# Kernel tuning notes

Measured on AMD Instinct MI355X. Metric: run time of the kernel, lower is better.

The kernel has to match this reference:

```python
import jax, jax.numpy as jnp
import numpy as np

B, L, V, D_MODEL = 1, 2048, 32000, 768
N_LAYER, D_STATE, EXPAND, D_CONV = 2, 16, 2, 4
D_INNER = EXPAND * D_MODEL            # 1536
DT_RANK = -(-D_MODEL // D_STATE)      # ceil(768/16) = 48
EPS = 1e-5


def setup_inputs() -> dict:
    key = jax.random.key(0)
    ks = jax.random.split(key, 12)
    s = 0.02
    inp = {
        "input_ids": jax.random.randint(ks[0], (B, L), 0, V),
        "emb": jax.random.normal(ks[1], (V, D_MODEL), jnp.float32) * s,
        "norm_w": jnp.ones((N_LAYER, D_MODEL), jnp.float32),
        "in_proj_w": jax.random.normal(ks[2], (N_LAYER, D_MODEL, 2 * D_INNER), jnp.float32) * s,
        "conv_w": jax.random.normal(ks[3], (N_LAYER, D_INNER, 1, D_CONV), jnp.float32) * s,
        "conv_b": jnp.zeros((N_LAYER, D_INNER), jnp.float32),
        "x_proj_w": jax.random.normal(ks[4], (N_LAYER, D_INNER, DT_RANK + 2 * D_STATE), jnp.float32) * s,
        "dt_proj_w": jax.random.normal(ks[5], (N_LAYER, DT_RANK, D_INNER), jnp.float32) * s,
        "dt_proj_b": jax.random.normal(ks[6], (N_LAYER, D_INNER), jnp.float32) * s,
        "A_log": jnp.tile(jnp.log(jnp.arange(1, D_STATE + 1, dtype=jnp.float32)), (N_LAYER, D_INNER, 1)),
        "D": jnp.ones((N_LAYER, D_INNER), jnp.float32),
        "out_proj_w": jax.random.normal(ks[7], (N_LAYER, D_INNER, D_MODEL), jnp.float32) * s,
    }
    return inp


def _rmsnorm(x, w):
    return x * jax.lax.rsqrt(jnp.mean(x * x, axis=-1, keepdims=True) + EPS) * w


def _selective_scan(u, delta, A, Bm, Cm, D):
    # u, delta: (b,l,d); A: (d,n); Bm, Cm: (b,l,n); D: (d,)
    deltaA = jnp.exp(delta[..., None] * A)                     # (b,l,d,n)
    dBu = delta[..., None] * Bm[:, :, None, :] * u[..., None]  # (b,l,d,n)

    def comb(c1, c2):
        a1, b1 = c1
        a2, b2 = c2
        return a2 * a1, a2 * b1 + b2

    _, h = jax.lax.associative_scan(comb, (deltaA, dBu), axis=1)
    y = jnp.einsum('bldn,bln->bld', h, Cm)
    return y + u * D


def _mamba_block(x, in_proj_w, conv_w, conv_b, x_proj_w, dt_proj_w, dt_proj_b, A_log, D, out_proj_w):
    # x: (b,l,d_model)
    xz = x @ in_proj_w                                  # (b,l,2*d_inner)
    xr, res = jnp.split(xz, 2, axis=-1)
    # causal depthwise conv1d (left pad d_conv-1)
    xc = jax.lax.conv_general_dilated(
        jnp.swapaxes(xr, 1, 2), conv_w, (1,), [(D_CONV - 1, 0)],
        feature_group_count=D_INNER,
        dimension_numbers=('NCH', 'OIH', 'NCH'))
    xr = jax.nn.silu(jnp.swapaxes(xc + conv_b[:, None], 1, 2))  # (b,l,d_inner)

    A = -jnp.exp(A_log)                                 # (d_inner, n)
    x_dbl = xr @ x_proj_w                               # (b,l,dt_rank+2n)
    dt, Bm, Cm = jnp.split(x_dbl, [DT_RANK, DT_RANK + D_STATE], axis=-1)
    delta = jax.nn.softplus(dt @ dt_proj_w + dt_proj_b) # (b,l,d_inner)
    y = _selective_scan(xr, delta, A, Bm, Cm, D)
    return (y * jax.nn.silu(res)) @ out_proj_w


def reference(input_ids, emb, norm_w, in_proj_w, conv_w, conv_b, x_proj_w,
              dt_proj_w, dt_proj_b, A_log, D, out_proj_w):
    x = emb[input_ids]                                  # (b,l,d_model)
    for i in range(N_LAYER):
        x = x + _mamba_block(_rmsnorm(x, norm_w[i]), in_proj_w[i], conv_w[i],
                             conv_b[i], x_proj_w[i], dt_proj_w[i], dt_proj_b[i],
                             A_log[i], D[i], out_proj_w[i])
    return x
```

## Files before the change

kernel.cpp:

```cpp
#include <hip/hip_runtime.h>
#include <math.h>

#define L_SEQ 2048
#define DM    768
#define DI    1536
#define DTR   48
#define DST   16
#define XDW   80
#define NCH   64
#define LC    32
#define XPS   8
#define XPK   (DI / XPS)

typedef short bf16x8 __attribute__((ext_vector_type(8)));
typedef float f32x4  __attribute__((ext_vector_type(4)));

__device__ __forceinline__ float silu_f(float x) {
    return x / (1.0f + __expf(-x));
}

__device__ __forceinline__ short f2bf(float x) {
    union { float f; unsigned u; } v; v.f = x;
    unsigned r = v.u + 0x7fff + ((v.u >> 16) & 1);
    return (short)(r >> 16);
}

__device__ __forceinline__ float bf2f(short s) {
    union { float f; unsigned u; } v;
    v.u = ((unsigned)(unsigned short)s) << 16;
    return v.f;
}

__global__ __launch_bounds__(256) void prep_kernel(
    const int*   __restrict__ ids,
    const float* __restrict__ emb,
    const float* __restrict__ norm_w,
    const float* __restrict__ in_proj_w,
    const float* __restrict__ out_proj_w,
    const float* __restrict__ x_proj_w,
    float* __restrict__ x,
    short* __restrict__ xn_bf,
    short* __restrict__ ipw_t, short* __restrict__ opw_t, short* __restrict__ xpw_t)
{
    __shared__ float tile[32 * 33];
    __shared__ float wred[4];
    const int tid = threadIdx.x;

    {
        int row = blockIdx.x;
        int tok = ids[row];
        float4 v4 = make_float4(0.f, 0.f, 0.f, 0.f);
        if (tid < DM / 4) {
            v4 = ((const float4*)emb)[(size_t)tok * (DM / 4) + tid];
            ((float4*)x)[(size_t)row * (DM / 4) + tid] = v4;
        }
        float s = v4.x * v4.x + v4.y * v4.y + v4.z * v4.z + v4.w * v4.w;
        #pragma unroll
        for (int off = 32; off > 0; off >>= 1) s += __shfl_down(s, off, 64);
        int wave = tid >> 6, lane = tid & 63;
        if (lane == 0) wred[wave] = s;
        __syncthreads();
        float tot = wred[0] + wred[1] + wred[2] + wred[3];
        float rs = rsqrtf(tot / (float)DM + 1e-5f);
        if (tid < DM / 4) {
            int i = tid * 4;
            short4 o;
            o.x = f2bf(v4.x * rs * norm_w[i + 0]);
            o.y = f2bf(v4.y * rs * norm_w[i + 1]);
            o.z = f2bf(v4.z * rs * norm_w[i + 2]);
            o.w = f2bf(v4.w * rs * norm_w[i + 3]);
            ((short4*)xn_bf)[(size_t)row * (DM / 4) + tid] = o;
        }
        __syncthreads();
    }

    int lx = tid & 31, ly = tid >> 5;
    for (int t = blockIdx.x; t < 7200; t += gridDim.x) {
        int layer = t >= 3600;
        int tt = t - layer * 3600;
        const float* src; short* dst; int K, N, txc;
        if (tt < 2304) {
            src = in_proj_w + (size_t)layer * DM * 2 * DI;
            dst = ipw_t + (size_t)layer * 2 * DI * DM;
            K = DM; N = 2 * DI; txc = 96;
        } else if (tt < 3456) {
            tt -= 2304;
            src = out_proj_w + (size_t)layer * DI * DM;
            dst = opw_t + (size_t)layer * DM * DI;
            K = DI; N = DM; txc = 24;
        } else {
            tt -= 3456;
            src = x_proj_w + (size_t)layer * DI * XDW;
            dst = xpw_t + (size_t)layer * XDW * DI;
            K = DI; N = XDW; txc = 3;
        }
        int n0 = (tt % txc) * 32, k0 = (tt / txc) * 32;
        __syncthreads();
        #pragma unroll
        for (int i = 0; i < 4; i++) {
            int nn = n0 + lx;
            tile[(ly + i * 8) * 33 + lx] =
                (nn < N) ? src[(size_t)(k0 + ly + i * 8) * N + nn] : 0.f;
        }
        __syncthreads();
        #pragma unroll
        for (int i = 0; i < 4; i++) {
            int nn = n0 + ly + i * 8;
            if (nn < N)
                dst[(size_t)nn * K + k0 + lx] = f2bf(tile[lx * 33 + ly + i * 8]);
        }
    }
}

__global__ __launch_bounds__(256) void rmsnorm_kernel(
    const float* __restrict__ x, const float* __restrict__ w,
    short* __restrict__ out)
{
    int row = blockIdx.x;
    const float* xr = x + (size_t)row * DM;
    float s = 0.f;
    for (int i = threadIdx.x; i < DM; i += 256) { float v = xr[i]; s += v * v; }
    #pragma unroll
    for (int off = 32; off > 0; off >>= 1) s += __shfl_down(s, off, 64);
    __shared__ float ws[4];
    int wave = threadIdx.x >> 6, lane = threadIdx.x & 63;
    if (lane == 0) ws[wave] = s;
    __syncthreads();
    float tot = ws[0] + ws[1] + ws[2] + ws[3];
    float rs = rsqrtf(tot / (float)DM + 1e-5f);
    for (int i = threadIdx.x; i < DM; i += 256)
        out[(size_t)row * DM + i] = f2bf(xr[i] * rs * w[i]);
}

__global__ __launch_bounds__(256) void gemm_inproj(
    const short* __restrict__ A, const short* __restrict__ Bt,
    short* __restrict__ xcz_bf, short* __restrict__ res_bf, int M, int N, int K)
{
    __shared__ short As[128 * 32];
    __shared__ short Bs[128 * 32];
    int tid = threadIdx.x, lane = tid & 63, w = tid >> 6;
    int wr = w >> 1, wc = w & 1;
    int brow = blockIdx.y * 128, bcol = blockIdx.x * 128;

    f32x4 acc[4][4] = {};

    for (int k0 = 0; k0 < K; k0 += 32) {
        #pragma unroll
        for (int i = 0; i < 2; i++) {
            int c = tid + i * 256;
            int r = c >> 2, q = c & 3;
            const short* ga = A  + (size_t)(brow + r) * K + k0 + q * 8;
            const short* gb = Bt + (size_t)(bcol + r) * K + k0 + q * 8;
            __builtin_amdgcn_global_load_lds(
                (const __attribute__((address_space(1))) void*)ga,
                (__attribute__((address_space(3))) void*)&As[r * 32 + q * 8],
                16, 0, 0);
            __builtin_amdgcn_global_load_lds(
                (const __attribute__((address_space(1))) void*)gb,
                (__attribute__((address_space(3))) void*)&Bs[r * 32 + q * 8],
                16, 0, 0);
        }
        __syncthreads();

        bf16x8 af[4], bfv[4];
        int kh = (lane >> 4) * 8;
        int ml = lane & 15;
        #pragma unroll
        for (int t = 0; t < 4; t++) {
            af[t]  = *(const bf16x8*)&As[(wr * 64 + t * 16 + ml) * 32 + kh];
            bfv[t] = *(const bf16x8*)&Bs[(wc * 64 + t * 16 + ml) * 32 + kh];
        }
        #pragma unroll
        for (int mt = 0; mt < 4; mt++)
            #pragma unroll
            for (int nt = 0; nt < 4; nt++)
                acc[mt][nt] = __builtin_amdgcn_mfma_f32_16x16x32_bf16(
                    af[mt], bfv[nt], acc[mt][nt], 0, 0, 0);
        __syncthreads();
    }

    short* dst  = (bcol < DI) ? xcz_bf : res_bf;
    int    cofs = (bcol < DI) ? bcol : (bcol - DI);
    int r0 = (lane >> 4) * 4, c0 = lane & 15;
    #pragma unroll
    for (int mt = 0; mt < 4; mt++)
        #pragma unroll
        for (int nt = 0; nt < 4; nt++)
            #pragma unroll
            for (int reg = 0; reg < 4; reg++) {
                int row = brow + wr * 64 + mt * 16 + r0 + reg;
                int col = cofs + wc * 64 + nt * 16 + c0;
                dst[(size_t)row * DI + col] = f2bf(acc[mt][nt][reg]);
            }
}

__global__ __launch_bounds__(256) void gemm_bf16_bt_n64(
    const short* __restrict__ A, const short* __restrict__ Bt,
    float* __restrict__ C, int M, int N, int K)
{
    __shared__ short As[128 * 32];
    __shared__ short Bs[64 * 32];
    int tid = threadIdx.x, lane = tid & 63, w = tid >> 6;
    int brow = blockIdx.y * 128, bcol = blockIdx.x * 64;

    f32x4 acc[2][4] = {};

    for (int k0 = 0; k0 < K; k0 += 32) {
        #pragma unroll
        for (int i = 0; i < 2; i++) {
            int c = tid + i * 256;
            int r = c >> 2, q = c & 3;
            const short* ga = A + (size_t)(brow + r) * K + k0 + q * 8;
            __builtin_amdgcn_global_load_lds(
                (const __attribute__((address_space(1))) void*)ga,
                (__attribute__((address_space(3))) void*)&As[r * 32 + q * 8],
                16, 0, 0);
        }
        {
            int r = tid >> 2, q = tid & 3;
            const short* gb = Bt + (size_t)(bcol + r) * K + k0 + q * 8;
            __builtin_amdgcn_global_load_lds(
                (const __attribute__((address_space(1))) void*)gb,
                (__attribute__((address_space(3))) void*)&Bs[r * 32 + q * 8],
                16, 0, 0);
        }
        __syncthreads();

        bf16x8 af[2], bfv[4];
        int kh = (lane >> 4) * 8;
        int ml = lane & 15;
        #pragma unroll
        for (int mt = 0; mt < 2; mt++)
            af[mt] = *(const bf16x8*)&As[(w * 32 + mt * 16 + ml) * 32 + kh];
        #pragma unroll
        for (int nt = 0; nt < 4; nt++)
            bfv[nt] = *(const bf16x8*)&Bs[(nt * 16 + ml) * 32 + kh];
        #pragma unroll
        for (int mt = 0; mt < 2; mt++)
            #pragma unroll
            for (int nt = 0; nt < 4; nt++)
                acc[mt][nt] = __builtin_amdgcn_mfma_f32_16x16x32_bf16(
                    af[mt], bfv[nt], acc[mt][nt], 0, 0, 0);
        __syncthreads();
    }

    int r0 = (lane >> 4) * 4, c0 = lane & 15;
    #pragma unroll
    for (int mt = 0; mt < 2; mt++)
        #pragma unroll
        for (int nt = 0; nt < 4; nt++)
            #pragma unroll
            for (int reg = 0; reg < 4; reg++) {
                int row = brow + w * 32 + mt * 16 + r0 + reg;
                int col = bcol + nt * 16 + c0;
                C[(size_t)row * N + col] += acc[mt][nt][reg];
            }
}

__global__ __launch_bounds__(256) void conv_silu_kernel(
    const short* __restrict__ xcz_bf, const float* __restrict__ w,
    const float* __restrict__ b, short* __restrict__ xr_bf)
{
    int idx = blockIdx.x * 256 + threadIdx.x;
    if (idx >= L_SEQ * DI) return;
    int l = idx / DI, c = idx % DI;
    float4 wc = ((const float4*)w)[c];
    const short* col = xcz_bf + c;
    float acc = b[c];
    if (l >= 3) {
        acc += wc.x * bf2f(col[(size_t)(l - 3) * DI])
             + wc.y * bf2f(col[(size_t)(l - 2) * DI])
             + wc.z * bf2f(col[(size_t)(l - 1) * DI])
             + wc.w * bf2f(col[(size_t)l * DI]);
    } else {
        const float wv[4] = {wc.x, wc.y, wc.z, wc.w};
        for (int k = 0; k < 4; k++) {
            int ls = l - 3 + k;
            if (ls >= 0) acc += wv[k] * bf2f(col[(size_t)ls * DI]);
        }
    }
    xr_bf[idx] = f2bf(silu_f(acc));
}

__global__ __launch_bounds__(256) void xproj_splitk(
    const short* __restrict__ xr_bf,
    const short* __restrict__ xpw_t,
    float* __restrict__ part)
{
    int w = threadIdx.x >> 6, lane = threadIdx.x & 63;
    int r0 = blockIdx.x * 64 + w * 16;
    int k0 = blockIdx.y * XPK;
    int ml = lane & 15, kh = (lane >> 4) * 8;

    f32x4 acc[5] = {};
    for (int ks = 0; ks < XPK; ks += 32) {
        bf16x8 a = *(const bf16x8*)&xr_bf[(size_t)(r0 + ml) * DI + k0 + ks + kh];
        #pragma unroll
        for (int t = 0; t < 5; t++) {
            bf16x8 b = *(const bf16x8*)&xpw_t[(size_t)(t * 16 + ml) * DI + k0 + ks + kh];
            acc[t] = __builtin_amdgcn_mfma_f32_16x16x32_bf16(a, b, acc[t], 0, 0, 0);
        }
    }
    float* po = part + (size_t)blockIdx.y * L_SEQ * XDW;
    int r_base = r0 + (lane >> 4) * 4;
    #pragma unroll
    for (int t = 0; t < 5; t++)
        #pragma unroll
        for (int reg = 0; reg < 4; reg++)
            po[(size_t)(r_base + reg) * XDW + t * 16 + ml] = acc[t][reg];
}

__global__ __launch_bounds__(256) void dtproj_fused(
    const float* __restrict__ xpart, const float* __restrict__ dpw,
    const float* __restrict__ dpb, float* __restrict__ delta,
    float* __restrict__ xdbl_bc)
{
    __shared__ __align__(16) float As_f[16 * 68];
    __shared__ __align__(16) float Bs_f[16 * 68];
    int tid = threadIdx.x;
    int ty = tid >> 4, tx = tid & 15;
    int t = blockIdx.x;
    int bcol = (t % 24) * 64;
    int brow = (t / 24) * 64;

    float acc[4][4] = {};
    for (int k0 = 0; k0 < 48; k0 += 16) {
        __syncthreads();
        #pragma unroll
        for (int i = 0; i < 4; i++) {
            int idx = tid + i * 256;
            int m = idx >> 4, k = idx & 15;
            float s = 0.f;
            #pragma unroll
            for (int p = 0; p < XPS; p++)
                s += xpart[((size_t)p * L_SEQ + brow + m) * XDW + k0 + k];
            As_f[k * 68 + m] = s;
        }
        #pragma unroll
        for (int i = 0; i < 4; i++) {
            int idx = tid + i * 256;
            int k = idx >> 6, n = idx & 63;
            Bs_f[k * 68 + n] = dpw[(size_t)(k0 + k) * DI + bcol + n];
        }
        __syncthreads();
        #pragma unroll
        for (int k = 0; k < 16; k++) {
            float4 av = *(const float4*)&As_f[k * 68 + ty * 4];
            float4 bv = *(const float4*)&Bs_f[k * 68 + tx * 4];
            float a4[4] = {av.x, av.y, av.z, av.w};
            float b4[4] = {bv.x, bv.y, bv.z, bv.w};
            #pragma unroll
            for (int i = 0; i < 4; i++)
                #pragma unroll
                for (int jj = 0; jj < 4; jj++)
                    acc[i][jj] += a4[i] * b4[jj];
        }
    }
    #pragma unroll
    for (int i = 0; i < 4; i++) {
        int row = brow + ty * 4 + i;
        #pragma unroll
        for (int jj = 0; jj < 4; jj++) {
            int col = bcol + tx * 4 + jj;
            float v = acc[i][jj] + dpb[col];
            delta[(size_t)row * DI + col] = (v > 20.f) ? v : log1pf(__expf(v));
        }
    }
    if (t % 24 == 0) {
        for (int e = tid; e < 64 * 32; e += 256) {
            int r = e >> 5, cc = e & 31;
            float s = 0.f;
            #pragma unroll
            for (int p = 0; p < XPS; p++)
                s += xpart[((size_t)p * L_SEQ + brow + r) * XDW + DTR + cc];
            xdbl_bc[(size_t)(brow + r) * 32 + cc] = s;
        }
    }
}

__global__ __launch_bounds__(256) void scan_passA(
    const float* __restrict__ delta, const short* __restrict__ xr_bf,
    const float* __restrict__ xdbl_bc, const float* __restrict__ al,
    float* __restrict__ aprod, float* __restrict__ hfin)
{
    int d = blockIdx.x * 256 + threadIdx.x;
    int c = blockIdx.y;

    float Aloc[DST], h[DST], P[DST];
    #pragma unroll
    for (int n4 = 0; n4 < DST; n4 += 4) {
        float4 alv = *(const float4*)&al[(size_t)d * DST + n4];
        Aloc[n4 + 0] = -__expf(alv.x); Aloc[n4 + 1] = -__expf(alv.y);
        Aloc[n4 + 2] = -__expf(alv.z); Aloc[n4 + 3] = -__expf(alv.w);
    }
    #pragma unroll
    for (int n = 0; n < DST; n++) { h[n] = 0.f; P[n] = 1.f; }

    int l0 = c * LC;
    for (int l = l0; l < l0 + LC; l++) {
        float dl = delta[(size_t)l * DI + d];
        float ul = bf2f(xr_bf[(size_t)l * DI + d]);
        float du = dl * ul;
        float Bv[DST];
        const float4* B4 = (const float4*)(xdbl_bc + (size_t)l * 32);
        *(float4*)&Bv[0] = B4[0]; *(float4*)&Bv[4]  = B4[1];
        *(float4*)&Bv[8] = B4[2]; *(float4*)&Bv[12] = B4[3];
        #pragma unroll
        for (int n = 0; n < DST; n++) {
            float da = __expf(dl * Aloc[n]);
            h[n] = h[n] * da + du * Bv[n];
            P[n] *= da;
        }
    }
    size_t base = ((size_t)c * DI + d) * DST;
    #pragma unroll
    for (int n = 0; n < DST; n += 4) {
        *(float4*)&aprod[base + n] = *(float4*)&P[n];
        *(float4*)&hfin[base + n]  = *(float4*)&h[n];
    }
}

__global__ __launch_bounds__(256) void scan_passB(
    const float* __restrict__ aprod, const float* __restrict__ hfin,
    float* __restrict__ hin)
{
    int idx = blockIdx.x * 256 + threadIdx.x;
    if (idx >= DI * DST) return;
    float cur = 0.f;
    for (int c = 0; c < NCH; c++) {
        size_t o = (size_t)c * DI * DST + idx;
        hin[o] = cur;
        cur = hfin[o] + aprod[o] * cur;
    }
}

__global__ __launch_bounds__(256) void scan_passC(
    const float* __restrict__ delta, const short* __restrict__ xr_bf,
    const float* __restrict__ xdbl_bc, const float* __restrict__ al,
    const float* __restrict__ dpp, const float* __restrict__ hin,
    const short* __restrict__ res_bf, short* __restrict__ y2)
{
    int d = blockIdx.x * 256 + threadIdx.x;
    int c = blockIdx.y;

    float Aloc[DST], h[DST];
    #pragma unroll
    for (int n4 = 0; n4 < DST; n4 += 4) {
        float4 alv = *(const float4*)&al[(size_t)d * DST + n4];
        Aloc[n4 + 0] = -__expf(alv.x); Aloc[n4 + 1] = -__expf(alv.y);
        Aloc[n4 + 2] = -__expf(alv.z); Aloc[n4 + 3] = -__expf(alv.w);
    }
    size_t base = ((size_t)c * DI + d) * DST;
    #pragma unroll
    for (int n = 0; n < DST; n += 4)
        *(float4*)&h[n] = *(const float4*)&hin[base + n];
    float Dd = dpp[d];

    int l0 = c * LC;
    for (int l = l0; l < l0 + LC; l++) {
        float dl = delta[(size_t)l * DI + d];
        float ul = bf2f(xr_bf[(size_t)l * DI + d]);
        float du = dl * ul;
        float Bv[DST], Cv[DST];
        const float4* B4 = (const float4*)(xdbl_bc + (size_t)l * 32);
        const float4* C4 = (const float4*)(xdbl_bc + (size_t)l * 32 + 16);
        *(float4*)&Bv[0] = B4[0]; *(float4*)&Bv[4]  = B4[1];
        *(float4*)&Bv[8] = B4[2]; *(float4*)&Bv[12] = B4[3];
        *(float4*)&Cv[0] = C4[0]; *(float4*)&Cv[4]  = C4[1];
        *(float4*)&Cv[8] = C4[2]; *(float4*)&Cv[12] = C4[3];
        float y = 0.f;
        #pragma unroll
        for (int n = 0; n < DST; n++) {
            float da = __expf(dl * Aloc[n]);
            h[n] = h[n] * da + du * Bv[n];
            y += h[n] * Cv[n];
        }
        y += ul * Dd;
        float r = bf2f(res_bf[(size_t)l * DI + d]);
        y2[(size_t)l * DI + d] = f2bf(y * silu_f(r));
    }
}

extern "C" void kernel_launch(void* const* d_in, const int* in_sizes, int n_in,
                              void* d_out, int out_size, void* d_ws, size_t ws_size,
                              hipStream_t stream)
{
    const int*   ids       = (const int*)d_in[0];
    const float* emb       = (const float*)d_in[1];
    const float* norm_w    = (const float*)d_in[2];
    const float* in_proj_w = (const float*)d_in[3];
    const float* conv_w    = (const float*)d_in[4];
    const float* conv_b    = (const float*)d_in[5];
    const float* x_proj_w  = (const float*)d_in[6];
    const float* dt_proj_w = (const float*)d_in[7];
    const float* dt_proj_b = (const float*)d_in[8];
    const float* A_log     = (const float*)d_in[9];
    const float* Dp        = (const float*)d_in[10];
    const float* out_proj_w= (const float*)d_in[11];

    float* x = (float*)d_out;

    char* wsb = (char*)d_ws;
    auto alloc_f = [&](size_t n) { float* p = (float*)wsb; wsb += n * 4; return p; };
    auto alloc_s = [&](size_t n) { short* p = (short*)wsb; wsb += ((n * 2 + 15) & ~15ull); return p; };

    float* delta   = alloc_f((size_t)L_SEQ * DI);
    float* xpart   = alloc_f((size_t)XPS * L_SEQ * XDW);
    float* xdbl_bc = alloc_f((size_t)L_SEQ * 32);
    float* aprod   = alloc_f((size_t)NCH * DI * DST);
    float* hfin    = alloc_f((size_t)NCH * DI * DST);
    float* hin     = alloc_f((size_t)NCH * DI * DST);
    short* xcz_bf  = alloc_s((size_t)L_SEQ * DI);
    short* res_bf  = alloc_s((size_t)L_SEQ * DI);
    short* xn_bf   = alloc_s((size_t)L_SEQ * DM);
    short* y2_bf   = alloc_s((size_t)L_SEQ * DI);
    short* xr_bf   = alloc_s((size_t)L_SEQ * DI);
    short* ipw_t   = alloc_s((size_t)2 * 2 * DI * DM);
    short* opw_t   = alloc_s((size_t)2 * DM * DI);
    short* xpw_t   = alloc_s((size_t)2 * XDW * DI);

    prep_kernel<<<L_SEQ, 256, 0, stream>>>(
        ids, emb, norm_w, in_proj_w, out_proj_w, x_proj_w,
        x, xn_bf, ipw_t, opw_t, xpw_t);

    for (int layer = 0; layer < 2; layer++) {
        const float* nw   = norm_w    + (size_t)layer * DM;
        const float* cw   = conv_w    + (size_t)layer * DI * 4;
        const float* cb   = conv_b    + (size_t)layer * DI;
        const float* dpw  = dt_proj_w + (size_t)layer * DTR * DI;
        const float* dpb  = dt_proj_b + (size_t)layer * DI;
        const float* al   = A_log     + (size_t)layer * DI * DST;
        const float* dpp  = Dp        + (size_t)layer * DI;
        const short* ipwt = ipw_t + (size_t)layer * 2 * DI * DM;
        const short* opwt = opw_t + (size_t)layer * DM * DI;
        const short* xpwt = xpw_t + (size_t)layer * XDW * DI;

        if (layer == 1)
            rmsnorm_kernel<<<L_SEQ, 256, 0, stream>>>(x, nw, xn_bf);

        gemm_inproj<<<dim3(2 * DI / 128, L_SEQ / 128), 256, 0, stream>>>(
            xn_bf, ipwt, xcz_bf, res_bf, L_SEQ, 2 * DI, DM);

        conv_silu_kernel<<<(L_SEQ * DI) / 256, 256, 0, stream>>>(
            xcz_bf, cw, cb, xr_bf);

        xproj_splitk<<<dim3(L_SEQ / 64, XPS), 256, 0, stream>>>(xr_bf, xpwt, xpart);

        dtproj_fused<<<768, 256, 0, stream>>>(xpart, dpw, dpb, delta, xdbl_bc);

        scan_passA<<<dim3(DI / 256, NCH), 256, 0, stream>>>(
            delta, xr_bf, xdbl_bc, al, aprod, hfin);
        scan_passB<<<(DI * DST) / 256, 256, 0, stream>>>(aprod, hfin, hin);
        scan_passC<<<dim3(DI / 256, NCH), 256, 0, stream>>>(
            delta, xr_bf, xdbl_bc, al, dpp, hin, res_bf, y2_bf);

        gemm_bf16_bt_n64<<<dim3(DM / 64, L_SEQ / 128), 256, 0, stream>>>(
            y2_bf, opwt, x, L_SEQ, DM, DI);
    }
}
```

Measured before the change: 468.4 us.

## Shrink GEMM tiles, split-K out_proj with atomics, fold scan pass B into pass C

The in_proj GEMM now uses 128x64 tiles instead of 128x128, doubling its block count. The out_proj GEMM is split along K into two halves that accumulate into the residual with atomic adds, raising its parallelism from 192 blocks. The separate chunk-carry kernel (scan_passB) is removed: each pass C block recomputes its initial state by walking all earlier chunks' products and final states. This saves a launch and the hin buffer, but costs redundant O(NCH) reads per block and makes out_proj accumulation order nondeterministic.

```diff
diff --git a/kernel.cpp b/kernel.cpp
--- a/kernel.cpp
+++ b/kernel.cpp
@@ -132,71 +132,9 @@
         out[(size_t)row * DM + i] = f2bf(xr[i] * rs * w[i]);
 }
 
-__global__ __launch_bounds__(256) void gemm_inproj(
+__global__ __launch_bounds__(256) void gemm_inproj64(
     const short* __restrict__ A, const short* __restrict__ Bt,
     short* __restrict__ xcz_bf, short* __restrict__ res_bf, int M, int N, int K)
-{
-    __shared__ short As[128 * 32];
-    __shared__ short Bs[128 * 32];
-    int tid = threadIdx.x, lane = tid & 63, w = tid >> 6;
-    int wr = w >> 1, wc = w & 1;
-    int brow = blockIdx.y * 128, bcol = blockIdx.x * 128;
-
-    f32x4 acc[4][4] = {};
-
-    for (int k0 = 0; k0 < K; k0 += 32) {
-        #pragma unroll
-        for (int i = 0; i < 2; i++) {
-            int c = tid + i * 256;
-            int r = c >> 2, q = c & 3;
-            const short* ga = A  + (size_t)(brow + r) * K + k0 + q * 8;
-            const short* gb = Bt + (size_t)(bcol + r) * K + k0 + q * 8;
-            __builtin_amdgcn_global_load_lds(
-                (const __attribute__((address_space(1))) void*)ga,
-                (__attribute__((address_space(3))) void*)&As[r * 32 + q * 8],
-                16, 0, 0);
-            __builtin_amdgcn_global_load_lds(
-                (const __attribute__((address_space(1))) void*)gb,
-                (__attribute__((address_space(3))) void*)&Bs[r * 32 + q * 8],
-                16, 0, 0);
-        }
-        __syncthreads();
-
-        bf16x8 af[4], bfv[4];
-        int kh = (lane >> 4) * 8;
-        int ml = lane & 15;
-        #pragma unroll
-        for (int t = 0; t < 4; t++) {
-            af[t]  = *(const bf16x8*)&As[(wr * 64 + t * 16 + ml) * 32 + kh];
-            bfv[t] = *(const bf16x8*)&Bs[(wc * 64 + t * 16 + ml) * 32 + kh];
-        }
-        #pragma unroll
-        for (int mt = 0; mt < 4; mt++)
-            #pragma unroll
-            for (int nt = 0; nt < 4; nt++)
-                acc[mt][nt] = __builtin_amdgcn_mfma_f32_16x16x32_bf16(
-                    af[mt], bfv[nt], acc[mt][nt], 0, 0, 0);
-        __syncthreads();
-    }
-
-    short* dst  = (bcol < DI) ? xcz_bf : res_bf;
-    int    cofs = (bcol < DI) ? bcol : (bcol - DI);
-    int r0 = (lane >> 4) * 4, c0 = lane & 15;
-    #pragma unroll
-    for (int mt = 0; mt < 4; mt++)
-        #pragma unroll
-        for (int nt = 0; nt < 4; nt++)
-            #pragma unroll
-            for (int reg = 0; reg < 4; reg++) {
-                int row = brow + wr * 64 + mt * 16 + r0 + reg;
-                int col = cofs + wc * 64 + nt * 16 + c0;
-                dst[(size_t)row * DI + col] = f2bf(acc[mt][nt][reg]);
-            }
-}
-
-__global__ __launch_bounds__(256) void gemm_bf16_bt_n64(
-    const short* __restrict__ A, const short* __restrict__ Bt,
-    float* __restrict__ C, int M, int N, int K)
 {
     __shared__ short As[128 * 32];
     __shared__ short Bs[64 * 32];
@@ -244,6 +182,73 @@
         __syncthreads();
     }
 
+    short* dst  = (bcol < DI) ? xcz_bf : res_bf;
+    int    cofs = (bcol < DI) ? bcol : (bcol - DI);
+    int r0 = (lane >> 4) * 4, c0 = lane & 15;
+    #pragma unroll
+    for (int mt = 0; mt < 2; mt++)
+        #pragma unroll
+        for (int nt = 0; nt < 4; nt++)
+            #pragma unroll
+            for (int reg = 0; reg < 4; reg++) {
+                int row = brow + w * 32 + mt * 16 + r0 + reg;
+                int col = cofs + nt * 16 + c0;
+                dst[(size_t)row * DI + col] = f2bf(acc[mt][nt][reg]);
+            }
+}
+
+__global__ __launch_bounds__(256) void gemm_outproj64(
+    const short* __restrict__ A, const short* __restrict__ Bt,
+    float* __restrict__ C, int M, int N, int K)
+{
+    __shared__ short As[128 * 32];
+    __shared__ short Bs[64 * 32];
+    int tid = threadIdx.x, lane = tid & 63, w = tid >> 6;
+    int brow = blockIdx.y * 128, bcol = blockIdx.x * 64;
+    int kbase = blockIdx.z * (K / 2);
+    int kend  = kbase + K / 2;
+
+    f32x4 acc[2][4] = {};
+
+    for (int k0 = kbase; k0 < kend; k0 += 32) {
+        #pragma unroll
+        for (int i = 0; i < 2; i++) {
+            int c = tid + i * 256;
+            int r = c >> 2, q = c & 3;
+            const short* ga = A + (size_t)(brow + r) * K + k0 + q * 8;
+            __builtin_amdgcn_global_load_lds(
+                (const __attribute__((address_space(1))) void*)ga,
+                (__attribute__((address_space(3))) void*)&As[r * 32 + q * 8],
+                16, 0, 0);
+        }
+        {
+            int r = tid >> 2, q = tid & 3;
+            const short* gb = Bt + (size_t)(bcol + r) * K + k0 + q * 8;
+            __builtin_amdgcn_global_load_lds(
+                (const __attribute__((address_space(1))) void*)gb,
+                (__attribute__((address_space(3))) void*)&Bs[r * 32 + q * 8],
+                16, 0, 0);
+        }
+        __syncthreads();
+
+        bf16x8 af[2], bfv[4];
+        int kh = (lane >> 4) * 8;
+        int ml = lane & 15;
+        #pragma unroll
+        for (int mt = 0; mt < 2; mt++)
+            af[mt] = *(const bf16x8*)&As[(w * 32 + mt * 16 + ml) * 32 + kh];
+        #pragma unroll
+        for (int nt = 0; nt < 4; nt++)
+            bfv[nt] = *(const bf16x8*)&Bs[(nt * 16 + ml) * 32 + kh];
+        #pragma unroll
+        for (int mt = 0; mt < 2; mt++)
+            #pragma unroll
+            for (int nt = 0; nt < 4; nt++)
+                acc[mt][nt] = __builtin_amdgcn_mfma_f32_16x16x32_bf16(
+                    af[mt], bfv[nt], acc[mt][nt], 0, 0, 0);
+        __syncthreads();
+    }
+
     int r0 = (lane >> 4) * 4, c0 = lane & 15;
     #pragma unroll
     for (int mt = 0; mt < 2; mt++)
@@ -253,7 +258,7 @@
             for (int reg = 0; reg < 4; reg++) {
                 int row = brow + w * 32 + mt * 16 + r0 + reg;
                 int col = bcol + nt * 16 + c0;
-                C[(size_t)row * N + col] += acc[mt][nt][reg];
+                unsafeAtomicAdd(&C[(size_t)row * N + col], acc[mt][nt][reg]);
             }
 }
 
@@ -420,24 +425,11 @@
     }
 }
 
-__global__ __launch_bounds__(256) void scan_passB(
-    const float* __restrict__ aprod, const float* __restrict__ hfin,
-    float* __restrict__ hin)
-{
-    int idx = blockIdx.x * 256 + threadIdx.x;
-    if (idx >= DI * DST) return;
-    float cur = 0.f;
-    for (int c = 0; c < NCH; c++) {
-        size_t o = (size_t)c * DI * DST + idx;
-        hin[o] = cur;
-        cur = hfin[o] + aprod[o] * cur;
-    }
-}
-
 __global__ __launch_bounds__(256) void scan_passC(
     const float* __restrict__ delta, const short* __restrict__ xr_bf,
     const float* __restrict__ xdbl_bc, const float* __restrict__ al,
-    const float* __restrict__ dpp, const float* __restrict__ hin,
+    const float* __restrict__ dpp,
+    const float* __restrict__ aprod, const float* __restrict__ hfin,
     const short* __restrict__ res_bf, short* __restrict__ y2)
 {
     int d = blockIdx.x * 256 + threadIdx.x;
@@ -450,12 +442,23 @@
         Aloc[n4 + 0] = -__expf(alv.x); Aloc[n4 + 1] = -__expf(alv.y);
         Aloc[n4 + 2] = -__expf(alv.z); Aloc[n4 + 3] = -__expf(alv.w);
     }
-    size_t base = ((size_t)c * DI + d) * DST;
-    #pragma unroll
-    for (int n = 0; n < DST; n += 4)
-        *(float4*)&h[n] = *(const float4*)&hin[base + n];
+    #pragma unroll
+    for (int n = 0; n < DST; n++) h[n] = 0.f;
+
+    for (int cp = 0; cp < c; cp++) {
+        size_t b2 = ((size_t)cp * DI + d) * DST;
+        float Pv[DST], Hv[DST];
+        #pragma unroll
+        for (int n = 0; n < DST; n += 4) {
+            *(float4*)&Pv[n] = *(const float4*)&aprod[b2 + n];
+            *(float4*)&Hv[n] = *(const float4*)&hfin[b2 + n];
+        }
+        #pragma unroll
+        for (int n = 0; n < DST; n++)
+            h[n] = Hv[n] + Pv[n] * h[n];
+    }
+
     float Dd = dpp[d];
-
     int l0 = c * LC;
     for (int l = l0; l < l0 + LC; l++) {
         float dl = delta[(size_t)l * DI + d];
@@ -509,7 +512,6 @@
     float* xdbl_bc = alloc_f((size_t)L_SEQ * 32);
     float* aprod   = alloc_f((size_t)NCH * DI * DST);
     float* hfin    = alloc_f((size_t)NCH * DI * DST);
-    float* hin     = alloc_f((size_t)NCH * DI * DST);
     short* xcz_bf  = alloc_s((size_t)L_SEQ * DI);
     short* res_bf  = alloc_s((size_t)L_SEQ * DI);
     short* xn_bf   = alloc_s((size_t)L_SEQ * DM);
@@ -538,7 +540,7 @@
         if (layer == 1)
             rmsnorm_kernel<<<L_SEQ, 256, 0, stream>>>(x, nw, xn_bf);
 
-        gemm_inproj<<<dim3(2 * DI / 128, L_SEQ / 128), 256, 0, stream>>>(
+        gemm_inproj64<<<dim3(2 * DI / 64, L_SEQ / 128), 256, 0, stream>>>(
             xn_bf, ipwt, xcz_bf, res_bf, L_SEQ, 2 * DI, DM);
 
         conv_silu_kernel<<<(L_SEQ * DI) / 256, 256, 0, stream>>>(
@@ -550,11 +552,10 @@
 
         scan_passA<<<dim3(DI / 256, NCH), 256, 0, stream>>>(
             delta, xr_bf, xdbl_bc, al, aprod, hfin);
-        scan_passB<<<(DI * DST) / 256, 256, 0, stream>>>(aprod, hfin, hin);
         scan_passC<<<dim3(DI / 256, NCH), 256, 0, stream>>>(
-            delta, xr_bf, xdbl_bc, al, dpp, hin, res_bf, y2_bf);
-
-        gemm_bf16_bt_n64<<<dim3(DM / 64, L_SEQ / 128), 256, 0, stream>>>(
+            delta, xr_bf, xdbl_bc, al, dpp, aprod, hfin, res_bf, y2_bf);
+
+        gemm_outproj64<<<dim3(DM / 64, L_SEQ / 128, 2), 256, 0, stream>>>(
             y2_bf, opwt, x, L_SEQ, DM, DI);
     }
 }
```

Result: slower. 500.0 us (+6.8%).
